# Kernel tuning notes

Measured on AMD Instinct MI355X. Metric: run time of the kernel, lower is better.

The kernel has to match this reference:

```python
import jax, jax.numpy as jnp
import numpy as np

B, N = 512, 256
SENTINEL = 256  # index value marking an unmatched keypoint


def setup_inputs() -> dict:
    key = jax.random.key(0)
    k1, k2, k3, k4, k5 = jax.random.split(key, 5)
    return {
        "src": jax.random.normal(k1, (B, 3, N), jnp.float32),
        "tgt": jax.random.normal(k2, (B, 3, N), jnp.float32),
        "scores": jax.random.normal(k3, (B, N, N), jnp.float32),
        "indices0": jax.random.randint(k4, (B, N), 0, 257, dtype=jnp.int32).astype(jnp.int64),
        "indices1": jax.random.randint(k5, (B, N), 0, 257, dtype=jnp.int32).astype(jnp.int64),
    }


def _forward(src, tgt, scores, indices0):
    # src, tgt: [B, 3, N]; scores: [B, N, N]; indices0: [B, N] int
    Bs, _, Np = src.shape
    dt = src.dtype
    S = jax.nn.softmax(scores, axis=2)                     # [B,N,N]
    m = jnp.where(indices0 == SENTINEL, -1, indices0)      # sentinel -> -1
    valid = m > -1                                         # [B,N]
    mc = jnp.clip(m, 0, Np - 1)                            # safe gather index
    kpts0 = src.transpose(0, 2, 1)                         # [B,N,3]
    kpts1 = tgt.transpose(0, 2, 1)                         # [B,N,3]
    # kpts1[matches[q]] for every q (masked later)
    tgt_g = jnp.take_along_axis(kpts1, mc[:, :, None], axis=1)      # [B,N,3]
    # Sg[b,p,q] = S[b, p, matches[b,q]]  (gathered columns)
    Sg = jnp.take_along_axis(S, mc[:, None, :], axis=2)             # [B,N,N]
    vmask = valid.astype(dt)
    vm = vmask[:, :, None]
    W = Sg * vmask[:, None, :]                              # zero out invalid match columns
    # weighted correspondence per (row) point p: c_p = sum_q W[p,q] * kpts1[m_q]
    c = jnp.einsum('bpq,bqd->bpd', W, tgt_g)                # [B,N,3]
    M = valid.sum(axis=1)                                   # [B] number of valid matches
    Minv = 1.0 / jnp.maximum(M, 1).astype(dt)
    mu0_v = (kpts0 * vm).sum(1) * Minv[:, None]             # mean of valid kpts0
    muc_v = (c * vm).sum(1) * Minv[:, None]                 # mean of valid correspondences
    Xv = (kpts0 - mu0_v[:, None, :]) * vm                   # centered + masked
    Yv = (c - muc_v[:, None, :]) * vm
    H_v = jnp.einsum('bnd,bne->bde', Xv, Yv)                # [B,3,3] cross-covariance
    # fallback branch (<= 3 valid matches): full soft correspondences, no mask
    c_f = jnp.einsum('bpq,bqd->bpd', S, kpts1)              # [B,N,3]
    mu0_f = kpts0.mean(1)
    muc_f = c_f.mean(1)
    H_f = jnp.einsum('bnd,bne->bde', kpts0 - mu0_f[:, None, :], c_f - muc_f[:, None, :])
    use_v = M > 3
    H = jnp.where(use_v[:, None, None], H_v, H_f)           # [B,3,3]
    mu = jnp.where(use_v[:, None], mu0_v, mu0_f)            # [B,3]
    # batched 3x3 Procrustes: R = V diag(1,1,det-sign) U^T
    u, s, vh = jnp.linalg.svd(H, full_matrices=False)
    v = vh.transpose(0, 2, 1)
    r0 = jnp.einsum('bij,bkj->bik', v, u)                   # V @ U^T
    flip = jnp.where(jnp.linalg.det(r0) < 0, -1.0, 1.0).astype(dt)
    scale = jnp.concatenate([jnp.ones((Bs, 2), dt), flip[:, None]], axis=1)
    v = v * scale[:, None, :]                               # flip last column (reflect)
    R = jnp.einsum('bij,bkj->bik', v, u)
    # NOTE: original code has a dangling `+src_corr.mean(...)` statement, so
    # t = -R @ mean(src_i) only (faithfully reproduced here).
    t = -jnp.einsum('bij,bj->bi', R, mu)                    # [B,3]
    return R, t


def reference(src, tgt, scores, indices0, indices1):
    return _forward(src, tgt, scores, indices0)
```

## Files before the change

kernel.cpp:

```cpp
#include <hip/hip_runtime.h>
#include <math.h>

#define BN 256
#define BLOCK 512

__device__ __forceinline__ float dpp_red63(float x) {
  x += __int_as_float(__builtin_amdgcn_update_dpp(0, __float_as_int(x), 0x111, 0xf, 0xf, true));
  x += __int_as_float(__builtin_amdgcn_update_dpp(0, __float_as_int(x), 0x112, 0xf, 0xf, true));
  x += __int_as_float(__builtin_amdgcn_update_dpp(0, __float_as_int(x), 0x114, 0xf, 0xf, true));
  x += __int_as_float(__builtin_amdgcn_update_dpp(0, __float_as_int(x), 0x118, 0xf, 0xf, true));
  x += __int_as_float(__builtin_amdgcn_update_dpp(0, __float_as_int(x), 0x142, 0xf, 0xf, true));
  x += __int_as_float(__builtin_amdgcn_update_dpp(0, __float_as_int(x), 0x143, 0xf, 0xf, true));
  return x;
}

__device__ __forceinline__ float bcast63(float x) {
  return __int_as_float(__builtin_amdgcn_readlane(__float_as_int(x), 63));
}

template<int P, int Q>
__device__ __forceinline__ void jrot(float K[3][3], float V[3][3]) {
  float apq = K[P][Q];
  if (apq == 0.f) return;
  float app = K[P][P], aqq = K[Q][Q];
  float tau = (aqq - app) / (2.f * apq);
  float st = sqrtf(1.f + tau * tau);
  float tt = (tau >= 0.f) ? 1.f / (tau + st) : 1.f / (tau - st);
  float c = 1.f / sqrtf(1.f + tt * tt);
  float s = tt * c;
#pragma unroll
  for (int k = 0; k < 3; k++) { float kp = K[k][P], kq = K[k][Q]; K[k][P] = c * kp - s * kq; K[k][Q] = s * kp + c * kq; }
#pragma unroll
  for (int k = 0; k < 3; k++) { float kp = K[P][k], kq = K[Q][k]; K[P][k] = c * kp - s * kq; K[Q][k] = s * kp + c * kq; }
#pragma unroll
  for (int k = 0; k < 3; k++) { float vp = V[k][P], vq = V[k][Q]; V[k][P] = c * vp - s * vq; V[k][Q] = s * vp + c * vq; }
}

template<int A, int C>
__device__ __forceinline__ void cswap(float lam[3], float V[3][3]) {
  if (lam[A] < lam[C]) {
    float tl = lam[A]; lam[A] = lam[C]; lam[C] = tl;
#pragma unroll
    for (int k = 0; k < 3; k++) { float tv = V[k][A]; V[k][A] = V[k][C]; V[k][C] = tv; }
  }
}

__device__ __forceinline__ void acc4(float4& T, float s, const float4& e) {
  T.x += s * e.x; T.y += s * e.y; T.z += s * e.z; T.w += s * e.w;
}

__device__ __forceinline__ float dot4(const float4& a, const float4& b) {
  return a.x * b.x + a.y * b.y + a.z * b.z + a.w * b.w;
}

extern "C" __global__ void __launch_bounds__(BLOCK, 2)
svdhead_kernel(const float* __restrict__ src,
               const float* __restrict__ tgt,
               const float* __restrict__ scores,
               const int* __restrict__ idx0,
               float* __restrict__ out)
{
  __shared__ __align__(16) float Af[6][BN];
  __shared__ __align__(16) float kxv[BN][4];
  __shared__ int cnt[BN];
  __shared__ float bacc[31];

  const int t = threadIdx.x;
  const int b = blockIdx.x;
  const int lane = t & 63;

  if (t < 31) bacc[t] = 0.f;
  if (t < BN) cnt[t] = 0;
  __syncthreads();

  float x0 = 0.f, x1 = 0.f, x2 = 0.f, vf = 0.f;
  if (t < BN) {
    int id = idx0[(size_t)b * BN + t];
    int valid = ((unsigned)id < 256u);
    vf = valid ? 1.f : 0.f;
    if (valid) atomicAdd(&cnt[id], 1);
    const float* sb = src + (size_t)b * 3 * BN;
    const float* tb = tgt + (size_t)b * 3 * BN;
    x0 = sb[t]; x1 = sb[BN + t]; x2 = sb[2 * BN + t];
    kxv[t][0] = x0; kxv[t][1] = x1; kxv[t][2] = x2; kxv[t][3] = vf;
    Af[3][t] = tb[t]; Af[4][t] = tb[BN + t]; Af[5][t] = tb[2 * BN + t];
  }
  {
    float rr[7];
    rr[0] = vf; rr[1] = vf * x0; rr[2] = vf * x1; rr[3] = vf * x2;
    rr[4] = x0; rr[5] = x1; rr[6] = x2;
#pragma unroll
    for (int k = 0; k < 7; k++) rr[k] = dpp_red63(rr[k]);
    if (lane == 63) {
      atomicAdd(&bacc[30], rr[0]);
      atomicAdd(&bacc[24], rr[1]); atomicAdd(&bacc[25], rr[2]); atomicAdd(&bacc[26], rr[3]);
      atomicAdd(&bacc[27], rr[4]); atomicAdd(&bacc[28], rr[5]); atomicAdd(&bacc[29], rr[6]);
    }
  }
  __syncthreads();
  if (t < BN) {
    float cf = (float)cnt[t];
    Af[0][t] = cf * Af[3][t];
    Af[1][t] = cf * Af[4][t];
    Af[2][t] = cf * Af[5][t];
  }
  __syncthreads();

  const int j0 = lane * 4;
  const int wave = t >> 6;
  const float* srow = scores + (size_t)b * BN * BN;
  const int pbase = wave * 32;
  const float* wbase = srow + (size_t)pbase * BN + j0;

  float4 Tv0 = {0,0,0,0}, Tv1 = {0,0,0,0}, Tv2 = {0,0,0,0}, Tv3 = {0,0,0,0};
  float4 Tf0 = {0,0,0,0}, Tf1 = {0,0,0,0}, Tf2 = {0,0,0,0}, Tf3 = {0,0,0,0};

  float4 cur[8];
#pragma unroll
  for (int r = 0; r < 8; r++) cur[r] = *(const float4*)(wbase + (size_t)r * BN);

#pragma unroll 1
  for (int g = 0; g < 4; g++) {
    const int gn = (g < 3) ? (g + 1) : 3;
    float4 nx[8];
#pragma unroll
    for (int r = 0; r < 8; r++)
      nx[r] = *(const float4*)(wbase + (size_t)(8 * gn + r) * BN);
    __builtin_amdgcn_sched_barrier(0);

    float s[8];
#pragma unroll
    for (int r = 0; r < 8; r++) {
      cur[r].x = __expf(cur[r].x); cur[r].y = __expf(cur[r].y);
      cur[r].z = __expf(cur[r].z); cur[r].w = __expf(cur[r].w);
      s[r] = (cur[r].x + cur[r].y) + (cur[r].z + cur[r].w);
    }
#pragma unroll
    for (int r = 0; r < 8; r++) s[r] = dpp_red63(s[r]);
#pragma unroll
    for (int r = 0; r < 8; r++) {
      float inv = __builtin_amdgcn_rcpf(bcast63(s[r]));
      float4 kv = *(const float4*)&kxv[pbase + 8 * g + r][0];
      float wf1 = inv * kv.x, wf2 = inv * kv.y, wf3 = inv * kv.z;
      float wv0 = kv.w * inv;
      float wv1 = kv.w * wf1, wv2 = kv.w * wf2, wv3 = kv.w * wf3;
      acc4(Tf0, inv, cur[r]);
      acc4(Tf1, wf1, cur[r]);
      acc4(Tf2, wf2, cur[r]);
      acc4(Tf3, wf3, cur[r]);
      acc4(Tv0, wv0, cur[r]);
      acc4(Tv1, wv1, cur[r]);
      acc4(Tv2, wv2, cur[r]);
      acc4(Tv3, wv3, cur[r]);
    }
#pragma unroll
    for (int r = 0; r < 8; r++) cur[r] = nx[r];
  }

  float acc[24];
  {
    float4 a6[6];
#pragma unroll
    for (int k = 0; k < 6; k++) a6[k] = *(const float4*)&Af[k][j0];
#pragma unroll
    for (int e = 0; e < 3; e++) {
      acc[0 + e]  = dot4(Tv1, a6[e]);
      acc[3 + e]  = dot4(Tv2, a6[e]);
      acc[6 + e]  = dot4(Tv3, a6[e]);
      acc[9 + e]  = dot4(Tf1, a6[3 + e]);
      acc[12 + e] = dot4(Tf2, a6[3 + e]);
      acc[15 + e] = dot4(Tf3, a6[3 + e]);
      acc[18 + e] = dot4(Tv0, a6[e]);
      acc[21 + e] = dot4(Tf0, a6[3 + e]);
    }
  }
#pragma unroll
  for (int k = 0; k < 24; k++) acc[k] = dpp_red63(acc[k]);
  if (lane == 63) {
#pragma unroll
    for (int k = 0; k < 24; k++) atomicAdd(&bacc[k], acc[k]);
  }
  __syncthreads();

  if (t == 0) {
    float M = bacc[30];
    float Minv = 1.f / fmaxf(M, 1.f);
    bool use_v = (M > 3.f);
    const float Ninv = 1.f / (float)BN;
    float H[3][3], mu[3];
#pragma unroll
    for (int d = 0; d < 3; d++) {
      mu[d] = use_v ? bacc[24 + d] * Minv : bacc[27 + d] * Ninv;
#pragma unroll
      for (int e = 0; e < 3; e++) {
        float hv = bacc[d * 3 + e]     - bacc[24 + d] * bacc[18 + e] * Minv;
        float hf = bacc[9 + d * 3 + e] - bacc[27 + d] * bacc[21 + e] * Ninv;
        H[d][e] = use_v ? hv : hf;
      }
    }
    float K[3][3];
#pragma unroll
    for (int i = 0; i < 3; i++)
#pragma unroll
      for (int j = 0; j < 3; j++) {
        float s_ = 0.f;
#pragma unroll
        for (int k = 0; k < 3; k++) s_ += H[k][i] * H[k][j];
        K[i][j] = s_;
      }
    float V[3][3] = {{1.f,0.f,0.f},{0.f,1.f,0.f},{0.f,0.f,1.f}};
    for (int sw = 0; sw < 8; sw++) { jrot<0,1>(K, V); jrot<0,2>(K, V); jrot<1,2>(K, V); }
    float lam[3] = {K[0][0], K[1][1], K[2][2]};
    cswap<0,1>(lam, V); cswap<1,2>(lam, V); cswap<0,1>(lam, V);

    float v1[3] = {V[0][0], V[1][0], V[2][0]};
    float v2[3] = {V[0][1], V[1][1], V[2][1]};
    float v3[3] = {V[0][2], V[1][2], V[2][2]};
    float u1[3], u2[3], u3[3];
#pragma unroll
    for (int i = 0; i < 3; i++) {
      u1[i] = H[i][0] * v1[0] + H[i][1] * v1[1] + H[i][2] * v1[2];
      u2[i] = H[i][0] * v2[0] + H[i][1] * v2[1] + H[i][2] * v2[2];
    }
    float n1s = u1[0]*u1[0] + u1[1]*u1[1] + u1[2]*u1[2];
    if (n1s > 1e-24f) { float r = 1.f / sqrtf(n1s); u1[0]*=r; u1[1]*=r; u1[2]*=r; }
    else { u1[0] = 1.f; u1[1] = 0.f; u1[2] = 0.f; }
    float d12 = u1[0]*u2[0] + u1[1]*u2[1] + u1[2]*u2[2];
    u2[0] -= d12 * u1[0]; u2[1] -= d12 * u1[1]; u2[2] -= d12 * u1[2];
    float n2s = u2[0]*u2[0] + u2[1]*u2[1] + u2[2]*u2[2];
    if (n2s > 1e-24f) { float r = 1.f / sqrtf(n2s); u2[0]*=r; u2[1]*=r; u2[2]*=r; }
    else {
      float ex_ = (fabsf(u1[0]) < 0.9f) ? 1.f : 0.f;
      float ey = 1.f - ex_;
      float cx = u1[1]*0.f - u1[2]*ey;
      float cy = u1[2]*ex_ - u1[0]*0.f;
      float cz = u1[0]*ey - u1[1]*ex_;
      float nn = 1.f / sqrtf(cx*cx + cy*cy + cz*cz + 1e-30f);
      u2[0] = cx*nn; u2[1] = cy*nn; u2[2] = cz*nn;
    }
    u3[0] = u1[1]*u2[2] - u1[2]*u2[1];
    u3[1] = u1[2]*u2[0] - u1[0]*u2[2];
    u3[2] = u1[0]*u2[1] - u1[1]*u2[0];
    float detV = v1[0]*(v2[1]*v3[2] - v2[2]*v3[1])
               - v1[1]*(v2[0]*v3[2] - v2[2]*v3[0])
               + v1[2]*(v2[0]*v3[1] - v2[1]*v3[0]);
    float f = (detV < 0.f) ? -1.f : 1.f;
    float R_[3][3];
#pragma unroll
    for (int i = 0; i < 3; i++)
#pragma unroll
      for (int k = 0; k < 3; k++)
        R_[i][k] = v1[i]*u1[k] + v2[i]*u2[k] + f * v3[i]*u3[k];

    float* Rout = out + (size_t)b * 9;
#pragma unroll
    for (int i = 0; i < 3; i++)
#pragma unroll
      for (int k = 0; k < 3; k++)
        Rout[i * 3 + k] = R_[i][k];
    float* Tout = out + (size_t)gridDim.x * 9 + (size_t)b * 3;
#pragma unroll
    for (int i = 0; i < 3; i++)
      Tout[i] = -(R_[i][0]*mu[0] + R_[i][1]*mu[1] + R_[i][2]*mu[2]);
  }
}

extern "C" void kernel_launch(void* const* d_in, const int* in_sizes, int n_in,
                              void* d_out, int out_size, void* d_ws, size_t ws_size,
                              hipStream_t stream) {
  const float* src = (const float*)d_in[0];
  const float* tgt = (const float*)d_in[1];
  const float* scores = (const float*)d_in[2];
  const int* idx0 = (const int*)d_in[3];
  float* out = (float*)d_out;
  int B = in_sizes[0] / (3 * BN);
  hipLaunchKernelGGL(svdhead_kernel, dim3(B), dim3(BLOCK), 0, stream,
                     src, tgt, scores, idx0, out);
}
```

Measured before the change: 52.10 us.

## Split each batch across four blocks and finalize SVD in a separate kernel

The single per-batch kernel becomes two. The first launches four 256-thread blocks per batch, each covering 64 score rows, and writes its partial moment sums to workspace. The second is a small kernel with one thread per batch that combines the partials and runs the 3x3 Jacobi SVD. This raises grid parallelism and keeps the serial single-thread SVD from stalling the block that streams scores. The cost is a second launch, a workspace round trip, and each block redoing the count histogram and tgt loads.

```diff
diff --git a/kernel.cpp b/kernel.cpp
--- a/kernel.cpp
+++ b/kernel.cpp
@@ -2,7 +2,8 @@
 #include <math.h>
 
 #define BN 256
-#define BLOCK 512
+#define RPC 64
+#define ABLOCK 256
 
 __device__ __forceinline__ float dpp_red63(float x) {
   x += __int_as_float(__builtin_amdgcn_update_dpp(0, __float_as_int(x), 0x111, 0xf, 0xf, true));
@@ -53,108 +54,125 @@
   return a.x * b.x + a.y * b.y + a.z * b.z + a.w * b.w;
 }
 
-extern "C" __global__ void __launch_bounds__(BLOCK, 2)
-svdhead_kernel(const float* __restrict__ src,
-               const float* __restrict__ tgt,
-               const float* __restrict__ scores,
-               const int* __restrict__ idx0,
-               float* __restrict__ out)
+extern "C" __global__ void __launch_bounds__(ABLOCK, 5)
+svd_partial(const float* __restrict__ src, const float* __restrict__ tgt,
+            const float* __restrict__ scores, const int* __restrict__ idx0,
+            float* __restrict__ ws)
 {
   __shared__ __align__(16) float Af[6][BN];
-  __shared__ __align__(16) float kxv[BN][4];
+  __shared__ __align__(16) float kxv[RPC][4];
+  __shared__ float vm[BN];
   __shared__ int cnt[BN];
-  __shared__ float bacc[31];
+  __shared__ float wsum[4][24];
 
   const int t = threadIdx.x;
-  const int b = blockIdx.x;
+  const int bc = blockIdx.x;
+  const int b = bc >> 2;
+  const int row0 = (bc & 3) * RPC;
   const int lane = t & 63;
-
-  if (t < 31) bacc[t] = 0.f;
-  if (t < BN) cnt[t] = 0;
+  const int wave = t >> 6;
+
+  cnt[t] = 0;
   __syncthreads();
 
-  float x0 = 0.f, x1 = 0.f, x2 = 0.f, vf = 0.f;
-  if (t < BN) {
-    int id = idx0[(size_t)b * BN + t];
+  {
+    int id = idx0[b * BN + t];
     int valid = ((unsigned)id < 256u);
-    vf = valid ? 1.f : 0.f;
+    vm[t] = valid ? 1.f : 0.f;
     if (valid) atomicAdd(&cnt[id], 1);
-    const float* sb = src + (size_t)b * 3 * BN;
     const float* tb = tgt + (size_t)b * 3 * BN;
-    x0 = sb[t]; x1 = sb[BN + t]; x2 = sb[2 * BN + t];
-    kxv[t][0] = x0; kxv[t][1] = x1; kxv[t][2] = x2; kxv[t][3] = vf;
     Af[3][t] = tb[t]; Af[4][t] = tb[BN + t]; Af[5][t] = tb[2 * BN + t];
   }
+  if (t < RPC) {
+    const float* sb = src + (size_t)b * 3 * BN + row0;
+    kxv[t][0] = sb[t]; kxv[t][1] = sb[BN + t]; kxv[t][2] = sb[2 * BN + t];
+  }
+  __syncthreads();
   {
-    float rr[7];
-    rr[0] = vf; rr[1] = vf * x0; rr[2] = vf * x1; rr[3] = vf * x2;
-    rr[4] = x0; rr[5] = x1; rr[6] = x2;
-#pragma unroll
-    for (int k = 0; k < 7; k++) rr[k] = dpp_red63(rr[k]);
-    if (lane == 63) {
-      atomicAdd(&bacc[30], rr[0]);
-      atomicAdd(&bacc[24], rr[1]); atomicAdd(&bacc[25], rr[2]); atomicAdd(&bacc[26], rr[3]);
-      atomicAdd(&bacc[27], rr[4]); atomicAdd(&bacc[28], rr[5]); atomicAdd(&bacc[29], rr[6]);
-    }
-  }
-  __syncthreads();
-  if (t < BN) {
     float cf = (float)cnt[t];
     Af[0][t] = cf * Af[3][t];
     Af[1][t] = cf * Af[4][t];
     Af[2][t] = cf * Af[5][t];
   }
+  if (t < RPC) kxv[t][3] = vm[row0 + t];
   __syncthreads();
 
+  if (wave == 0) {
+    float4 kv = *(const float4*)&kxv[lane][0];
+    float rr[7];
+    rr[0] = kv.w;
+    rr[1] = kv.w * kv.x; rr[2] = kv.w * kv.y; rr[3] = kv.w * kv.z;
+    rr[4] = kv.x; rr[5] = kv.y; rr[6] = kv.z;
+#pragma unroll
+    for (int k = 0; k < 7; k++) rr[k] = dpp_red63(rr[k]);
+    if (lane == 63) {
+      float* wp = ws + (size_t)bc * 32;
+      wp[30] = rr[0];
+      wp[24] = rr[1]; wp[25] = rr[2]; wp[26] = rr[3];
+      wp[27] = rr[4]; wp[28] = rr[5]; wp[29] = rr[6];
+    }
+  }
+
   const int j0 = lane * 4;
-  const int wave = t >> 6;
-  const float* srow = scores + (size_t)b * BN * BN;
-  const int pbase = wave * 32;
-  const float* wbase = srow + (size_t)pbase * BN + j0;
+  const float* wbase = scores + ((size_t)b * BN + row0 + wave * 16) * BN + j0;
 
   float4 Tv0 = {0,0,0,0}, Tv1 = {0,0,0,0}, Tv2 = {0,0,0,0}, Tv3 = {0,0,0,0};
   float4 Tf0 = {0,0,0,0}, Tf1 = {0,0,0,0}, Tf2 = {0,0,0,0}, Tf3 = {0,0,0,0};
 
-  float4 cur[8];
-#pragma unroll
-  for (int r = 0; r < 8; r++) cur[r] = *(const float4*)(wbase + (size_t)r * BN);
+  float4 c0 = *(const float4*)(wbase);
+  float4 c1 = *(const float4*)(wbase + (size_t)BN);
+  float4 c2 = *(const float4*)(wbase + (size_t)2 * BN);
+  float4 c3 = *(const float4*)(wbase + (size_t)3 * BN);
 
 #pragma unroll 1
   for (int g = 0; g < 4; g++) {
     const int gn = (g < 3) ? (g + 1) : 3;
-    float4 nx[8];
-#pragma unroll
-    for (int r = 0; r < 8; r++)
-      nx[r] = *(const float4*)(wbase + (size_t)(8 * gn + r) * BN);
+    float4 n0 = *(const float4*)(wbase + (size_t)(4 * gn) * BN);
+    float4 n1 = *(const float4*)(wbase + (size_t)(4 * gn + 1) * BN);
+    float4 n2 = *(const float4*)(wbase + (size_t)(4 * gn + 2) * BN);
+    float4 n3 = *(const float4*)(wbase + (size_t)(4 * gn + 3) * BN);
     __builtin_amdgcn_sched_barrier(0);
 
-    float s[8];
-#pragma unroll
-    for (int r = 0; r < 8; r++) {
-      cur[r].x = __expf(cur[r].x); cur[r].y = __expf(cur[r].y);
-      cur[r].z = __expf(cur[r].z); cur[r].w = __expf(cur[r].w);
-      s[r] = (cur[r].x + cur[r].y) + (cur[r].z + cur[r].w);
-    }
-#pragma unroll
-    for (int r = 0; r < 8; r++) s[r] = dpp_red63(s[r]);
-#pragma unroll
-    for (int r = 0; r < 8; r++) {
-      float inv = __builtin_amdgcn_rcpf(bcast63(s[r]));
-      float4 kv = *(const float4*)&kxv[pbase + 8 * g + r][0];
-      float wf1 = inv * kv.x, wf2 = inv * kv.y, wf3 = inv * kv.z;
-      float wv0 = kv.w * inv;
-      float wv1 = kv.w * wf1, wv2 = kv.w * wf2, wv3 = kv.w * wf3;
-      acc4(Tf0, inv, cur[r]);
-      acc4(Tf1, wf1, cur[r]);
-      acc4(Tf2, wf2, cur[r]);
-      acc4(Tf3, wf3, cur[r]);
-      acc4(Tv0, wv0, cur[r]);
-      acc4(Tv1, wv1, cur[r]);
-      acc4(Tv2, wv2, cur[r]);
-      acc4(Tv3, wv3, cur[r]);
-    }
-#pragma unroll
-    for (int r = 0; r < 8; r++) cur[r] = nx[r];
+    c0.x = __expf(c0.x); c0.y = __expf(c0.y); c0.z = __expf(c0.z); c0.w = __expf(c0.w);
+    c1.x = __expf(c1.x); c1.y = __expf(c1.y); c1.z = __expf(c1.z); c1.w = __expf(c1.w);
+    c2.x = __expf(c2.x); c2.y = __expf(c2.y); c2.z = __expf(c2.z); c2.w = __expf(c2.w);
+    c3.x = __expf(c3.x); c3.y = __expf(c3.y); c3.z = __expf(c3.z); c3.w = __expf(c3.w);
+    float s0 = (c0.x + c0.y) + (c0.z + c0.w);
+    float s1 = (c1.x + c1.y) + (c1.z + c1.w);
+    float s2 = (c2.x + c2.y) + (c2.z + c2.w);
+    float s3 = (c3.x + c3.y) + (c3.z + c3.w);
+    s0 = dpp_red63(s0); s1 = dpp_red63(s1); s2 = dpp_red63(s2); s3 = dpp_red63(s3);
+    float i0 = __builtin_amdgcn_rcpf(bcast63(s0));
+    float i1 = __builtin_amdgcn_rcpf(bcast63(s1));
+    float i2 = __builtin_amdgcn_rcpf(bcast63(s2));
+    float i3 = __builtin_amdgcn_rcpf(bcast63(s3));
+
+    const int pr = wave * 16 + 4 * g;
+    {
+      float4 kv = *(const float4*)&kxv[pr][0];
+      float wf1 = i0 * kv.x, wf2 = i0 * kv.y, wf3 = i0 * kv.z, wv0 = kv.w * i0;
+      acc4(Tf0, i0, c0);  acc4(Tf1, wf1, c0); acc4(Tf2, wf2, c0); acc4(Tf3, wf3, c0);
+      acc4(Tv0, wv0, c0); acc4(Tv1, kv.w * wf1, c0); acc4(Tv2, kv.w * wf2, c0); acc4(Tv3, kv.w * wf3, c0);
+    }
+    {
+      float4 kv = *(const float4*)&kxv[pr + 1][0];
+      float wf1 = i1 * kv.x, wf2 = i1 * kv.y, wf3 = i1 * kv.z, wv0 = kv.w * i1;
+      acc4(Tf0, i1, c1);  acc4(Tf1, wf1, c1); acc4(Tf2, wf2, c1); acc4(Tf3, wf3, c1);
+      acc4(Tv0, wv0, c1); acc4(Tv1, kv.w * wf1, c1); acc4(Tv2, kv.w * wf2, c1); acc4(Tv3, kv.w * wf3, c1);
+    }
+    {
+      float4 kv = *(const float4*)&kxv[pr + 2][0];
+      float wf1 = i2 * kv.x, wf2 = i2 * kv.y, wf3 = i2 * kv.z, wv0 = kv.w * i2;
+      acc4(Tf0, i2, c2);  acc4(Tf1, wf1, c2); acc4(Tf2, wf2, c2); acc4(Tf3, wf3, c2);
+      acc4(Tv0, wv0, c2); acc4(Tv1, kv.w * wf1, c2); acc4(Tv2, kv.w * wf2, c2); acc4(Tv3, kv.w * wf3, c2);
+    }
+    {
+      float4 kv = *(const float4*)&kxv[pr + 3][0];
+      float wf1 = i3 * kv.x, wf2 = i3 * kv.y, wf3 = i3 * kv.z, wv0 = kv.w * i3;
+      acc4(Tf0, i3, c3);  acc4(Tf1, wf1, c3); acc4(Tf2, wf2, c3); acc4(Tf3, wf3, c3);
+      acc4(Tv0, wv0, c3); acc4(Tv1, kv.w * wf1, c3); acc4(Tv2, kv.w * wf2, c3); acc4(Tv3, kv.w * wf3, c3);
+    }
+    c0 = n0; c1 = n1; c2 = n2; c3 = n3;
   }
 
   float acc[24];
@@ -178,91 +196,106 @@
   for (int k = 0; k < 24; k++) acc[k] = dpp_red63(acc[k]);
   if (lane == 63) {
 #pragma unroll
-    for (int k = 0; k < 24; k++) atomicAdd(&bacc[k], acc[k]);
+    for (int k = 0; k < 24; k++) wsum[wave][k] = acc[k];
   }
   __syncthreads();
-
-  if (t == 0) {
-    float M = bacc[30];
-    float Minv = 1.f / fmaxf(M, 1.f);
-    bool use_v = (M > 3.f);
-    const float Ninv = 1.f / (float)BN;
-    float H[3][3], mu[3];
-#pragma unroll
-    for (int d = 0; d < 3; d++) {
-      mu[d] = use_v ? bacc[24 + d] * Minv : bacc[27 + d] * Ninv;
-#pragma unroll
-      for (int e = 0; e < 3; e++) {
-        float hv = bacc[d * 3 + e]     - bacc[24 + d] * bacc[18 + e] * Minv;
-        float hf = bacc[9 + d * 3 + e] - bacc[27 + d] * bacc[21 + e] * Ninv;
-        H[d][e] = use_v ? hv : hf;
-      }
-    }
-    float K[3][3];
-#pragma unroll
-    for (int i = 0; i < 3; i++)
-#pragma unroll
-      for (int j = 0; j < 3; j++) {
-        float s_ = 0.f;
-#pragma unroll
-        for (int k = 0; k < 3; k++) s_ += H[k][i] * H[k][j];
-        K[i][j] = s_;
-      }
-    float V[3][3] = {{1.f,0.f,0.f},{0.f,1.f,0.f},{0.f,0.f,1.f}};
-    for (int sw = 0; sw < 8; sw++) { jrot<0,1>(K, V); jrot<0,2>(K, V); jrot<1,2>(K, V); }
-    float lam[3] = {K[0][0], K[1][1], K[2][2]};
-    cswap<0,1>(lam, V); cswap<1,2>(lam, V); cswap<0,1>(lam, V);
-
-    float v1[3] = {V[0][0], V[1][0], V[2][0]};
-    float v2[3] = {V[0][1], V[1][1], V[2][1]};
-    float v3[3] = {V[0][2], V[1][2], V[2][2]};
-    float u1[3], u2[3], u3[3];
-#pragma unroll
-    for (int i = 0; i < 3; i++) {
-      u1[i] = H[i][0] * v1[0] + H[i][1] * v1[1] + H[i][2] * v1[2];
-      u2[i] = H[i][0] * v2[0] + H[i][1] * v2[1] + H[i][2] * v2[2];
-    }
-    float n1s = u1[0]*u1[0] + u1[1]*u1[1] + u1[2]*u1[2];
-    if (n1s > 1e-24f) { float r = 1.f / sqrtf(n1s); u1[0]*=r; u1[1]*=r; u1[2]*=r; }
-    else { u1[0] = 1.f; u1[1] = 0.f; u1[2] = 0.f; }
-    float d12 = u1[0]*u2[0] + u1[1]*u2[1] + u1[2]*u2[2];
-    u2[0] -= d12 * u1[0]; u2[1] -= d12 * u1[1]; u2[2] -= d12 * u1[2];
-    float n2s = u2[0]*u2[0] + u2[1]*u2[1] + u2[2]*u2[2];
-    if (n2s > 1e-24f) { float r = 1.f / sqrtf(n2s); u2[0]*=r; u2[1]*=r; u2[2]*=r; }
-    else {
-      float ex_ = (fabsf(u1[0]) < 0.9f) ? 1.f : 0.f;
-      float ey = 1.f - ex_;
-      float cx = u1[1]*0.f - u1[2]*ey;
-      float cy = u1[2]*ex_ - u1[0]*0.f;
-      float cz = u1[0]*ey - u1[1]*ex_;
-      float nn = 1.f / sqrtf(cx*cx + cy*cy + cz*cz + 1e-30f);
-      u2[0] = cx*nn; u2[1] = cy*nn; u2[2] = cz*nn;
-    }
-    u3[0] = u1[1]*u2[2] - u1[2]*u2[1];
-    u3[1] = u1[2]*u2[0] - u1[0]*u2[2];
-    u3[2] = u1[0]*u2[1] - u1[1]*u2[0];
-    float detV = v1[0]*(v2[1]*v3[2] - v2[2]*v3[1])
-               - v1[1]*(v2[0]*v3[2] - v2[2]*v3[0])
-               + v1[2]*(v2[0]*v3[1] - v2[1]*v3[0]);
-    float f = (detV < 0.f) ? -1.f : 1.f;
-    float R_[3][3];
-#pragma unroll
-    for (int i = 0; i < 3; i++)
-#pragma unroll
-      for (int k = 0; k < 3; k++)
-        R_[i][k] = v1[i]*u1[k] + v2[i]*u2[k] + f * v3[i]*u3[k];
-
-    float* Rout = out + (size_t)b * 9;
-#pragma unroll
-    for (int i = 0; i < 3; i++)
-#pragma unroll
-      for (int k = 0; k < 3; k++)
-        Rout[i * 3 + k] = R_[i][k];
-    float* Tout = out + (size_t)gridDim.x * 9 + (size_t)b * 3;
-#pragma unroll
-    for (int i = 0; i < 3; i++)
-      Tout[i] = -(R_[i][0]*mu[0] + R_[i][1]*mu[1] + R_[i][2]*mu[2]);
-  }
+  if (t < 24) {
+    float v = (wsum[0][t] + wsum[1][t]) + (wsum[2][t] + wsum[3][t]);
+    ws[(size_t)bc * 32 + t] = v;
+  }
+}
+
+extern "C" __global__ void svd_finalize(const float* __restrict__ ws,
+                                        float* __restrict__ out, int NB)
+{
+  int b = blockIdx.x * blockDim.x + threadIdx.x;
+  if (b >= NB) return;
+  float s31[31];
+#pragma unroll
+  for (int k = 0; k < 31; k++) {
+    const float* wp = ws + (size_t)b * 4 * 32 + k;
+    s31[k] = (wp[0] + wp[32]) + (wp[64] + wp[96]);
+  }
+
+  float M = s31[30];
+  float Minv = 1.f / fmaxf(M, 1.f);
+  bool use_v = (M > 3.f);
+  const float Ninv = 1.f / (float)BN;
+  float H[3][3], mu[3];
+#pragma unroll
+  for (int d = 0; d < 3; d++) {
+    mu[d] = use_v ? s31[24 + d] * Minv : s31[27 + d] * Ninv;
+#pragma unroll
+    for (int e = 0; e < 3; e++) {
+      float hv = s31[d * 3 + e]     - s31[24 + d] * s31[18 + e] * Minv;
+      float hf = s31[9 + d * 3 + e] - s31[27 + d] * s31[21 + e] * Ninv;
+      H[d][e] = use_v ? hv : hf;
+    }
+  }
+  float K[3][3];
+#pragma unroll
+  for (int i = 0; i < 3; i++)
+#pragma unroll
+    for (int j = 0; j < 3; j++) {
+      float s_ = 0.f;
+#pragma unroll
+      for (int k = 0; k < 3; k++) s_ += H[k][i] * H[k][j];
+      K[i][j] = s_;
+    }
+  float V[3][3] = {{1.f,0.f,0.f},{0.f,1.f,0.f},{0.f,0.f,1.f}};
+  for (int sw = 0; sw < 8; sw++) { jrot<0,1>(K, V); jrot<0,2>(K, V); jrot<1,2>(K, V); }
+  float lam[3] = {K[0][0], K[1][1], K[2][2]};
+  cswap<0,1>(lam, V); cswap<1,2>(lam, V); cswap<0,1>(lam, V);
+
+  float v1[3] = {V[0][0], V[1][0], V[2][0]};
+  float v2[3] = {V[0][1], V[1][1], V[2][1]};
+  float v3[3] = {V[0][2], V[1][2], V[2][2]};
+  float u1[3], u2[3], u3[3];
+#pragma unroll
+  for (int i = 0; i < 3; i++) {
+    u1[i] = H[i][0] * v1[0] + H[i][1] * v1[1] + H[i][2] * v1[2];
+    u2[i] = H[i][0] * v2[0] + H[i][1] * v2[1] + H[i][2] * v2[2];
+  }
+  float n1s = u1[0]*u1[0] + u1[1]*u1[1] + u1[2]*u1[2];
+  if (n1s > 1e-24f) { float r = 1.f / sqrtf(n1s); u1[0]*=r; u1[1]*=r; u1[2]*=r; }
+  else { u1[0] = 1.f; u1[1] = 0.f; u1[2] = 0.f; }
+  float d12 = u1[0]*u2[0] + u1[1]*u2[1] + u1[2]*u2[2];
+  u2[0] -= d12 * u1[0]; u2[1] -= d12 * u1[1]; u2[2] -= d12 * u1[2];
+  float n2s = u2[0]*u2[0] + u2[1]*u2[1] + u2[2]*u2[2];
+  if (n2s > 1e-24f) { float r = 1.f / sqrtf(n2s); u2[0]*=r; u2[1]*=r; u2[2]*=r; }
+  else {
+    float ex_ = (fabsf(u1[0]) < 0.9f) ? 1.f : 0.f;
+    float ey = 1.f - ex_;
+    float cx = u1[1]*0.f - u1[2]*ey;
+    float cy = u1[2]*ex_ - u1[0]*0.f;
+    float cz = u1[0]*ey - u1[1]*ex_;
+    float nn = 1.f / sqrtf(cx*cx + cy*cy + cz*cz + 1e-30f);
+    u2[0] = cx*nn; u2[1] = cy*nn; u2[2] = cz*nn;
+  }
+  u3[0] = u1[1]*u2[2] - u1[2]*u2[1];
+  u3[1] = u1[2]*u2[0] - u1[0]*u2[2];
+  u3[2] = u1[0]*u2[1] - u1[1]*u2[0];
+  float detV = v1[0]*(v2[1]*v3[2] - v2[2]*v3[1])
+             - v1[1]*(v2[0]*v3[2] - v2[2]*v3[0])
+             + v1[2]*(v2[0]*v3[1] - v2[1]*v3[0]);
+  float f = (detV < 0.f) ? -1.f : 1.f;
+  float R_[3][3];
+#pragma unroll
+  for (int i = 0; i < 3; i++)
+#pragma unroll
+    for (int k = 0; k < 3; k++)
+      R_[i][k] = v1[i]*u1[k] + v2[i]*u2[k] + f * v3[i]*u3[k];
+
+  float* Rout = out + (size_t)b * 9;
+#pragma unroll
+  for (int i = 0; i < 3; i++)
+#pragma unroll
+    for (int k = 0; k < 3; k++)
+      Rout[i * 3 + k] = R_[i][k];
+  float* Tout = out + (size_t)NB * 9 + (size_t)b * 3;
+#pragma unroll
+  for (int i = 0; i < 3; i++)
+    Tout[i] = -(R_[i][0]*mu[0] + R_[i][1]*mu[1] + R_[i][2]*mu[2]);
 }
 
 extern "C" void kernel_launch(void* const* d_in, const int* in_sizes, int n_in,
@@ -273,7 +306,11 @@
   const float* scores = (const float*)d_in[2];
   const int* idx0 = (const int*)d_in[3];
   float* out = (float*)d_out;
-  int B = in_sizes[0] / (3 * BN);
-  hipLaunchKernelGGL(svdhead_kernel, dim3(B), dim3(BLOCK), 0, stream,
-                     src, tgt, scores, idx0, out);
-}
+  float* ws = (float*)d_ws;
+  int NB = in_sizes[0] / (3 * BN);
+
+  hipLaunchKernelGGL(svd_partial, dim3(NB * 4), dim3(ABLOCK), 0, stream,
+                     src, tgt, scores, idx0, ws);
+  hipLaunchKernelGGL(svd_finalize, dim3((NB + 255) / 256), dim3(256), 0, stream,
+                     ws, out, NB);
+}
```

Measured after the change: 71.01 us. +36.3%, slower.
